# Optimization experiments

Hardware: AMD Instinct MI355X
Metric: run time of the kernel (lower is better)

The kernel has to match this reference:

```python
import jax, jax.numpy as jnp
import numpy as np

E = 2048      # enc_size
B = 64        # number of output buffer slices (leaves)
STEPS = 2 * B - 1  # 63 reduces then 64 shifts


def _res(x, W, b):
    # ResLayer: residual + ReLU MLP, x: (E,)
    return x + jax.nn.relu(x @ W + b)


def setup_inputs() -> dict:
    key = jax.random.key(0)
    ks = jax.random.split(key, 12)
    s = 1.0 / np.sqrt(E)
    inp = {
        "input_encoding": jax.random.normal(ks[0], (E,), dtype=jnp.float32),
        # 63 ones (reduce) followed by 64 zeros (shift): valid shift-reduce tree
        "fixed_actions": jnp.concatenate([jnp.ones((B - 1,), jnp.int64 if jax.config.jax_enable_x64 else jnp.int32),
                                          jnp.zeros((B,), jnp.int64 if jax.config.jax_enable_x64 else jnp.int32)]),
        # act_scorer: ResLayer + Linear(E, 2)
        "act_res_W": jax.random.normal(ks[1], (E, E), jnp.float32) * s,
        "act_res_b": jnp.zeros((E,), jnp.float32),
        "act_W": jax.random.normal(ks[2], (E, 2), jnp.float32) * s,
        "act_b": jnp.zeros((2,), jnp.float32),
        # unreduce_l: two ResLayers
        "ul1_W": jax.random.normal(ks[3], (E, E), jnp.float32) * s,
        "ul1_b": jnp.zeros((E,), jnp.float32),
        "ul2_W": jax.random.normal(ks[4], (E, E), jnp.float32) * s,
        "ul2_b": jnp.zeros((E,), jnp.float32),
        # unreduce_r: two ResLayers
        "ur1_W": jax.random.normal(ks[5], (E, E), jnp.float32) * s,
        "ur1_b": jnp.zeros((E,), jnp.float32),
        "ur2_W": jax.random.normal(ks[6], (E, E), jnp.float32) * s,
        "ur2_b": jnp.zeros((E,), jnp.float32),
    }
    return inp


def reference(input_encoding, act_res_W, act_res_b, act_W, act_b,
              ul1_W, ul1_b, ul2_W, ul2_b, ur1_W, ur1_b, ur2_W, ur2_b,
              fixed_actions):
    # fixed_actions is a constant action sequence -> Python-level unroll of the
    # data-dependent stack machine (faithful to the torch while-loop).
    acts = np.asarray(fixed_actions)
    stack = [input_encoding]
    buffer_slices = []
    logit_rec = []
    for step in range(acts.shape[0]):
        a = int(acts[step])
        top = stack[-1]
        logits = _res(top, act_res_W, act_res_b) @ act_W + act_b  # (2,)
        score = jax.nn.softmax(logits)[a]
        st = 1.0 + score - jax.lax.stop_gradient(score)  # straight-through scale (fwd == 1)
        logit_rec.append(logits)
        if a == 0:  # shift: pop to buffer
            x = stack.pop()
            buffer_slices.append(x * st)
            if len(stack) == 0:
                break
        else:  # reduce: pop, push unreduce_r then unreduce_l
            prev = stack.pop()
            l = _res(_res(prev, ul1_W, ul1_b), ul2_W, ul2_b)
            r = _res(_res(prev, ur1_W, ur1_b), ur2_W, ur2_b)
            stack.append(r * st)
            stack.append(l * st)
    return jnp.stack(buffer_slices, 0), jnp.stack(logit_rec, 0)
```

## Files before the change

kernel.cpp:

```cpp
#include <hip/hip_runtime.h>

#define EN 2048
#define NCH 256
#define CTH 1024
#define SENT 0xFFFFFFFFu

#define T_OFF    0
#define H_OFF    (64 * EN)
#define FLG_OFF  (128 * EN)
#define HT_OFF   (129 * EN)
#define P_OFF    (256 * EN)

#define AL64(p)   __hip_atomic_load((const unsigned long long*)(p), __ATOMIC_RELAXED, __HIP_MEMORY_SCOPE_AGENT)
#define AL32(p)   __hip_atomic_load((const unsigned*)(p), __ATOMIC_RELAXED, __HIP_MEMORY_SCOPE_AGENT)
#define AS32(p,v) __hip_atomic_store((unsigned*)(p), (v), __ATOMIC_RELAXED, __HIP_MEMORY_SCOPE_AGENT)
#define AS64(p,v) __hip_atomic_store((unsigned long long*)(p), (v), __ATOMIC_RELAXED, __HIP_MEMORY_SCOPE_AGENT)

__device__ __forceinline__ float af(unsigned u) { return __uint_as_float(u); }
__device__ __forceinline__ unsigned long long pk(float a, float b) {
    return ((unsigned long long)__float_as_uint(b) << 32) | __float_as_uint(a);
}

__device__ __forceinline__ void done_bar(unsigned* D, int b, int tid) {
    __syncthreads();
    if (tid < 64) {
        if (tid == 0) {
            asm volatile("s_waitcnt vmcnt(0)" ::: "memory");
            AS32(&D[b], 1u);
        }
        const unsigned long long* f = (const unsigned long long*)D;
        const unsigned long long GOOD = 0x0000000100000001ULL;
        for (long it = 0; it < 200000000L; ++it) {
            unsigned long long a = AL64(&f[tid * 2]);
            unsigned long long c = AL64(&f[tid * 2 + 1]);
            if (!__any((int)(a != GOOD || c != GOOD))) break;
        }
    }
    __syncthreads();
}

template<int NKT>
__device__ __forceinline__ void gemm_phase(
    const float* __restrict__ a_stage_row,
    const float* __restrict__ W, int kbase, int c0,
    float* __restrict__ Pslot, int tid, float* __restrict__ GB)
{
    const int kq  = tid >> 8;
    const int rem = tid & 255;
    const int ar  = rem >> 2;
    const int ak8 = (rem & 3) * 8;
    const int wk  = rem >> 3;
    const int wc  = (rem & 7) * 8;
    const int tr  = rem >> 4;
    const int tc  = rem & 15;
    float* As = GB + kq * (2 * 32 * 68);
    float* Wt = As + 32 * 68;

    float4 a0 = {0,0,0,0}, a1 = {0,0,0,0}, a2 = {0,0,0,0}, a3 = {0,0,0,0};

    unsigned long long ra0, ra1, ra2, ra3;
    float4 rw0, rw1;
    {
        ra0 = AL64(a_stage_row + kbase + ak8);
        ra1 = AL64(a_stage_row + kbase + ak8 + 2);
        ra2 = AL64(a_stage_row + kbase + ak8 + 4);
        ra3 = AL64(a_stage_row + kbase + ak8 + 6);
        const float* wp = W + (size_t)(kbase + wk) * EN + c0 + wc;
        rw0 = *(const float4*)wp; rw1 = *(const float4*)(wp + 4);
    }
    for (int kt = 0; kt < NKT; ++kt) {
        __syncthreads();
        As[(ak8+0)*68+ar] = af((unsigned)ra0); As[(ak8+1)*68+ar] = af((unsigned)(ra0>>32));
        As[(ak8+2)*68+ar] = af((unsigned)ra1); As[(ak8+3)*68+ar] = af((unsigned)(ra1>>32));
        As[(ak8+4)*68+ar] = af((unsigned)ra2); As[(ak8+5)*68+ar] = af((unsigned)(ra2>>32));
        As[(ak8+6)*68+ar] = af((unsigned)ra3); As[(ak8+7)*68+ar] = af((unsigned)(ra3>>32));
        *(float4*)&Wt[wk*68+wc]     = rw0;
        *(float4*)&Wt[wk*68+wc+4]  = rw1;
        __syncthreads();
        if (kt + 1 < NKT) {
            int kb = kbase + (kt + 1) * 32;
            ra0 = AL64(a_stage_row + kb + ak8);
            ra1 = AL64(a_stage_row + kb + ak8 + 2);
            ra2 = AL64(a_stage_row + kb + ak8 + 4);
            ra3 = AL64(a_stage_row + kb + ak8 + 6);
            const float* wp = W + (size_t)(kb + wk) * EN + c0 + wc;
            rw0 = *(const float4*)wp; rw1 = *(const float4*)(wp + 4);
        }
#pragma unroll
        for (int kk = 0; kk < 32; ++kk) {
            float4 av = *(const float4*)&As[kk*68 + tr*4];
            float4 wv = *(const float4*)&Wt[kk*68 + tc*4];
            a0.x += av.x*wv.x; a0.y += av.x*wv.y; a0.z += av.x*wv.z; a0.w += av.x*wv.w;
            a1.x += av.y*wv.x; a1.y += av.y*wv.y; a1.z += av.y*wv.z; a1.w += av.y*wv.w;
            a2.x += av.z*wv.x; a2.y += av.z*wv.y; a2.z += av.z*wv.z; a2.w += av.z*wv.w;
            a3.x += av.w*wv.x; a3.y += av.w*wv.y; a3.z += av.w*wv.z; a3.w += av.w*wv.w;
        }
    }
    __syncthreads();
    if (kq > 0) {
        float* d = GB + (kq - 1) * 4096 + rem;
        d[0*256]=a0.x; d[1*256]=a0.y; d[2*256]=a0.z;  d[3*256]=a0.w;
        d[4*256]=a1.x; d[5*256]=a1.y; d[6*256]=a1.z;  d[7*256]=a1.w;
        d[8*256]=a2.x; d[9*256]=a2.y; d[10*256]=a2.z; d[11*256]=a2.w;
        d[12*256]=a3.x; d[13*256]=a3.y; d[14*256]=a3.z; d[15*256]=a3.w;
    }
    __syncthreads();
    if (kq == 0) {
#pragma unroll
        for (int q = 0; q < 3; ++q) {
            const float* s = GB + q * 4096 + rem;
            a0.x+=s[0*256]; a0.y+=s[1*256]; a0.z+=s[2*256];  a0.w+=s[3*256];
            a1.x+=s[4*256]; a1.y+=s[5*256]; a1.z+=s[6*256];  a1.w+=s[7*256];
            a2.x+=s[8*256]; a2.y+=s[9*256]; a2.z+=s[10*256]; a2.w+=s[11*256];
            a3.x+=s[12*256]; a3.y+=s[13*256]; a3.z+=s[14*256]; a3.w+=s[15*256];
        }
        float* p0 = Pslot + (size_t)(tr*4    ) * EN + c0 + tc*4;
        float* p1 = Pslot + (size_t)(tr*4 + 1) * EN + c0 + tc*4;
        float* p2 = Pslot + (size_t)(tr*4 + 2) * EN + c0 + tc*4;
        float* p3 = Pslot + (size_t)(tr*4 + 3) * EN + c0 + tc*4;
        AS64(p0, pk(a0.x, a0.y)); AS64(p0 + 2, pk(a0.z, a0.w));
        AS64(p1, pk(a1.x, a1.y)); AS64(p1 + 2, pk(a1.z, a1.w));
        AS64(p2, pk(a2.x, a2.y)); AS64(p2 + 2, pk(a2.z, a2.w));
        AS64(p3, pk(a3.x, a3.y)); AS64(p3 + 2, pk(a3.z, a3.w));
    }
    __syncthreads();
}

__global__ __launch_bounds__(CTH, 1) void mega_kernel(
    const float* __restrict__ x0,
    const float* __restrict__ ul1W, const float* __restrict__ ul1b,
    const float* __restrict__ ul2W, const float* __restrict__ ul2b,
    const float* __restrict__ ur1W, const float* __restrict__ ur1b,
    const float* __restrict__ ur2W, const float* __restrict__ ur2b,
    const float* __restrict__ arW,  const float* __restrict__ arb,
    const float* __restrict__ aW,   const float* __restrict__ ab,
    float* __restrict__ T, float* __restrict__ Hb, float* __restrict__ RT1,
    float* __restrict__ HT, float* __restrict__ P, unsigned* __restrict__ FLG,
    float* __restrict__ out)
{
    __shared__ __align__(16) float xs[EN];
    __shared__ __align__(16) float red_t[16][20];
    __shared__ float bias_s[16];
    __shared__ __align__(16) float GB[4 * 2 * 32 * 68];
    __shared__ float lred[16][2];

    const int tid  = threadIdx.x;
    const int b    = blockIdx.x;
    const int lane = tid & 63;
    const int wv   = tid >> 6;

    {
        const int half  = b >> 7;
        const int idx   = b & 127;
        const int c0    = idx * 16;
        const int col   = tid & 15;
        const int chunk = tid >> 4;
        const float* Wg = half ? ul2W : ul1W;
        const float* bg = half ? ul2b : ul1b;

        float4 w[8];
#pragma unroll
        for (int j = 0; j < 8; ++j) {
            const float* wp = Wg + (size_t)(chunk * 32 + j * 4) * EN + c0 + col;
            w[j].x = wp[0]; w[j].y = wp[EN]; w[j].z = wp[2 * EN]; w[j].w = wp[3 * EN];
        }
        if (tid < 16) bias_s[tid] = bg[c0 + tid];

        for (int k = 1; k <= 63; ++k) {
            if (half == 0 && k == 1) {
                reinterpret_cast<float2*>(xs)[tid] = reinterpret_cast<const float2*>(x0)[tid];
            } else {
                const float* src = half ? (Hb + (size_t)k * EN) : (T + (size_t)(k - 1) * EN);
                const unsigned long long* s64 =
                    reinterpret_cast<const unsigned long long*>(src) + (size_t)wv * 64 + lane;
                unsigned long long v;
                for (;;) {
                    v = AL64(s64);
                    unsigned lo = (unsigned)v, hi = (unsigned)(v >> 32);
                    if (!__any((int)(lo == SENT || hi == SENT))) break;
                }
                float2 xv;
                xv.x = af((unsigned)v); xv.y = af((unsigned)(v >> 32));
                reinterpret_cast<float2*>(xs)[tid] = xv;
            }
            __syncthreads();

            float s = 0.f;
            const float4* xv4 = reinterpret_cast<const float4*>(xs) + chunk * 8;
#pragma unroll
            for (int j = 0; j < 8; ++j) {
                float4 x4 = xv4[j];
                s += x4.x * w[j].x + x4.y * w[j].y + x4.z * w[j].z + x4.w * w[j].w;
            }
            s += __shfl_xor(s, 16, 64);
            s += __shfl_xor(s, 32, 64);
            if (lane < 16) red_t[lane][wv] = s;
            __syncthreads();

            if (wv == 0 && lane < 16) {
                float4 r0 = *(const float4*)&red_t[lane][0];
                float4 r1 = *(const float4*)&red_t[lane][4];
                float4 r2 = *(const float4*)&red_t[lane][8];
                float4 r3 = *(const float4*)&red_t[lane][12];
                float tot = ((r0.x + r0.y) + (r0.z + r0.w)) + ((r1.x + r1.y) + (r1.z + r1.w))
                          + ((r2.x + r2.y) + (r2.z + r2.w)) + ((r3.x + r3.y) + (r3.z + r3.w))
                          + bias_s[lane];
                float o = xs[c0 + lane] + fmaxf(tot, 0.f);
                float* dst = half ? (T + (size_t)k * EN) : (Hb + (size_t)k * EN);
                AS32(&dst[c0 + lane], __float_as_uint(o));
                if (half && k == 63) out[c0 + lane] = o;
                if (!half && k == 1) AS32(&T[c0 + lane], __float_as_uint(xs[c0 + lane]));
            }
        }
    }

    unsigned* D0 = FLG;            unsigned* D1 = FLG + 256;
    unsigned* D2 = FLG + 512;      unsigned* D3 = FLG + 768;
    unsigned* D4 = FLG + 1024;     unsigned* D5 = FLG + 1280;

    {
        const int rem = tid & 255, kq = tid >> 8;
        int ar = rem >> 2; if (ar > 62) ar = 62;
        int cc = b & 31, ks = b >> 5;
        gemm_phase<2>(T + (size_t)ar * EN, ur1W, ks * 256 + kq * 64, cc * 64,
                      P + (size_t)ks * 64 * EN, tid, GB);
    }
    done_bar(D0, b, tid);

    if (tid < 504) {
        int m = tid >> 3, c = 8 * b + (tid & 7);
        float p = 0.f;
#pragma unroll
        for (int ks = 0; ks < 8; ++ks) p += af(AL32(P + ((size_t)ks * 64 + m) * EN + c));
        float tv = af(AL32(T + (size_t)m * EN + c));
        AS32(RT1 + (size_t)m * EN + c, __float_as_uint(tv + fmaxf(p + ur1b[c], 0.f)));
    }
    done_bar(D1, b, tid);

    {
        const int rem = tid & 255, kq = tid >> 8;
        int ar = rem >> 2; if (ar > 62) ar = 62;
        int cc = b & 31, ks = b >> 5;
        gemm_phase<2>(RT1 + (size_t)ar * EN, ur2W, ks * 256 + kq * 64, cc * 64,
                      P + (size_t)ks * 64 * EN, tid, GB);
    }
    done_bar(D2, b, tid);

    if (tid < 504) {
        int m = tid >> 3, c = 8 * b + (tid & 7);
        float p = 0.f;
#pragma unroll
        for (int ks = 0; ks < 8; ++ks) p += af(AL32(P + ((size_t)ks * 64 + m) * EN + c));
        float rv = af(AL32(RT1 + (size_t)m * EN + c));
        AS32(out + (size_t)(63 - m) * EN + c, __float_as_uint(rv + fmaxf(p + ur2b[c], 0.f)));
    }
    done_bar(D3, b, tid);

    {
        const int rem = tid & 255, kq = tid >> 8;
        int cc = b & 31, mh = (b >> 5) & 1, ks = b >> 6;
        int rp = mh * 64 + (rem >> 2); if (rp > 126) rp = 126;
        const float* arow = (rp <= 63) ? (T + (size_t)rp * EN) : (out + (size_t)(rp - 63) * EN);
        gemm_phase<4>(arow, arW, ks * 512 + kq * 128, cc * 64,
                      P + (size_t)(ks * 2 + mh) * 64 * EN, tid, GB);
    }
    done_bar(D4, b, tid);

    if (tid < 1016) {
        int m = tid >> 3, c = 8 * b + (tid & 7);
        int mh = m >> 6, mr = m & 63;
        float p = 0.f;
#pragma unroll
        for (int ks = 0; ks < 4; ++ks) p += af(AL32(P + ((size_t)(ks * 2 + mh) * 64 + mr) * EN + c));
        float tv = (m <= 63) ? af(AL32(T + (size_t)m * EN + c))
                             : af(AL32(out + (size_t)(m - 63) * EN + c));
        AS32(HT + (size_t)m * EN + c, __float_as_uint(tv + fmaxf(p + arb[c], 0.f)));
    }
    done_bar(D5, b, tid);

    if (b < 127) {
        const float* h = HT + (size_t)b * EN;
        unsigned long long hv = AL64(h + tid * 2);
        float h0 = af((unsigned)hv), h1 = af((unsigned)(hv >> 32));
        float4 w4 = *(const float4*)(aW + (size_t)tid * 4);
        float s0 = h0 * w4.x + h1 * w4.z;
        float s1 = h0 * w4.y + h1 * w4.w;
#pragma unroll
        for (int off = 32; off; off >>= 1) { s0 += __shfl_down(s0, off, 64); s1 += __shfl_down(s1, off, 64); }
        if (lane == 0) { lred[wv][0] = s0; lred[wv][1] = s1; }
        __syncthreads();
        if (tid == 0) {
            float t0 = ab[0], t1 = ab[1];
#pragma unroll
            for (int q = 0; q < 16; ++q) { t0 += lred[q][0]; t1 += lred[q][1]; }
            out[64 * EN + b * 2]     = t0;
            out[64 * EN + b * 2 + 1] = t1;
        }
    }
}

extern "C" void kernel_launch(void* const* d_in, const int* in_sizes, int n_in,
                              void* d_out, int out_size, void* d_ws, size_t ws_size,
                              hipStream_t stream)
{
    const float* x0   = (const float*)d_in[0];
    const float* arW  = (const float*)d_in[2];
    const float* arb  = (const float*)d_in[3];
    const float* aW   = (const float*)d_in[4];
    const float* ab   = (const float*)d_in[5];
    const float* ul1W = (const float*)d_in[6];
    const float* ul1b = (const float*)d_in[7];
    const float* ul2W = (const float*)d_in[8];
    const float* ul2b = (const float*)d_in[9];
    const float* ur1W = (const float*)d_in[10];
    const float* ur1b = (const float*)d_in[11];
    const float* ur2W = (const float*)d_in[12];
    const float* ur2b = (const float*)d_in[13];

    float* ws  = (float*)d_ws;
    float* out = (float*)d_out;
    float* T   = ws + T_OFF;
    float* Hb  = ws + H_OFF;
    float* RT1 = ws + H_OFF;
    float* HT  = ws + HT_OFF;
    float* P   = ws + P_OFF;
    unsigned* FLG = (unsigned*)(ws + FLG_OFF);

    hipMemsetAsync(ws, 0xFF, (size_t)(129 * EN) * sizeof(float), stream);

    void* args[] = { (void*)&x0, (void*)&ul1W, (void*)&ul1b, (void*)&ul2W, (void*)&ul2b,
                     (void*)&ur1W, (void*)&ur1b, (void*)&ur2W, (void*)&ur2b,
                     (void*)&arW, (void*)&arb, (void*)&aW, (void*)&ab,
                     (void*)&T, (void*)&Hb, (void*)&RT1, (void*)&HT, (void*)&P,
                     (void*)&FLG, (void*)&out };
    hipError_t err = hipLaunchCooperativeKernel(reinterpret_cast<void*>(mega_kernel),
                                                dim3(NCH), dim3(CTH), args, 0, stream);
    if (err != hipSuccess) {
        (void)hipGetLastError();
        mega_kernel<<<dim3(NCH), dim3(CTH), 0, stream>>>(
            x0, ul1W, ul1b, ul2W, ul2b, ur1W, ur1b, ur2W, ur2b,
            arW, arb, aW, ab, T, Hb, RT1, HT, P, FLG, out);
    }
}
```

Measured before the change: 359.0 us.

## Replace per-step syncthreads with LDS counter wait and vectorize cross-block loads

The serial unreduce_l chain now drops both per-step __syncthreads: waves bump a workgroup-scope LDS counter and only wave 0 spins on it before doing the final reduction, cutting barrier cost on the 63-step critical path. The split-K epilogue phases switch from scalar 32-bit atomic loads and stores to 16-byte loads and stores through inline asm with sc1, using fewer threads. The GEMM staging drops its register prefetch in favour of direct dwordx4 loads followed by a waitcnt. Risks include a race on xs reuse without a barrier, and the loss of load/compute overlap in the GEMM.

```diff
diff --git a/kernel.cpp b/kernel.cpp
--- a/kernel.cpp
+++ b/kernel.cpp
@@ -4,6 +4,9 @@
 #define NCH 256
 #define CTH 1024
 #define SENT 0xFFFFFFFFu
+
+typedef float f32x4 __attribute__((ext_vector_type(4)));
+typedef float f32x2 __attribute__((ext_vector_type(2)));
 
 #define T_OFF    0
 #define H_OFF    (64 * EN)
@@ -12,22 +15,18 @@
 #define P_OFF    (256 * EN)
 
 #define AL64(p)   __hip_atomic_load((const unsigned long long*)(p), __ATOMIC_RELAXED, __HIP_MEMORY_SCOPE_AGENT)
-#define AL32(p)   __hip_atomic_load((const unsigned*)(p), __ATOMIC_RELAXED, __HIP_MEMORY_SCOPE_AGENT)
 #define AS32(p,v) __hip_atomic_store((unsigned*)(p), (v), __ATOMIC_RELAXED, __HIP_MEMORY_SCOPE_AGENT)
-#define AS64(p,v) __hip_atomic_store((unsigned long long*)(p), (v), __ATOMIC_RELAXED, __HIP_MEMORY_SCOPE_AGENT)
+
+#define GL16(d, p) asm volatile("global_load_dwordx4 %0, %1, off sc1" : "=&v"(d) : "v"(p) : "memory")
+#define ST16(p, d) asm volatile("global_store_dwordx4 %0, %1, off sc1" :: "v"(p), "v"(d) : "memory")
 
 __device__ __forceinline__ float af(unsigned u) { return __uint_as_float(u); }
-__device__ __forceinline__ unsigned long long pk(float a, float b) {
-    return ((unsigned long long)__float_as_uint(b) << 32) | __float_as_uint(a);
-}
 
 __device__ __forceinline__ void done_bar(unsigned* D, int b, int tid) {
+    asm volatile("s_waitcnt vmcnt(0)" ::: "memory");
     __syncthreads();
     if (tid < 64) {
-        if (tid == 0) {
-            asm volatile("s_waitcnt vmcnt(0)" ::: "memory");
-            AS32(&D[b], 1u);
-        }
+        if (tid == 0) AS32(&D[b], 1u);
         const unsigned long long* f = (const unsigned long long*)D;
         const unsigned long long GOOD = 0x0000000100000001ULL;
         for (long it = 0; it < 200000000L; ++it) {
@@ -40,88 +39,70 @@
 }
 
 template<int NKT>
-__device__ __forceinline__ void gemm_phase(
-    const float* __restrict__ a_stage_row,
+__device__ __forceinline__ void gemm64(
+    const float* __restrict__ Arow,
     const float* __restrict__ W, int kbase, int c0,
     float* __restrict__ Pslot, int tid, float* __restrict__ GB)
 {
     const int kq  = tid >> 8;
     const int rem = tid & 255;
-    const int ar  = rem >> 2;
+    const int am  = rem >> 2;
     const int ak8 = (rem & 3) * 8;
     const int wk  = rem >> 3;
-    const int wc  = (rem & 7) * 8;
-    const int tr  = rem >> 4;
-    const int tc  = rem & 15;
-    float* As = GB + kq * (2 * 32 * 68);
-    float* Wt = As + 32 * 68;
-
-    float4 a0 = {0,0,0,0}, a1 = {0,0,0,0}, a2 = {0,0,0,0}, a3 = {0,0,0,0};
-
-    unsigned long long ra0, ra1, ra2, ra3;
-    float4 rw0, rw1;
-    {
-        ra0 = AL64(a_stage_row + kbase + ak8);
-        ra1 = AL64(a_stage_row + kbase + ak8 + 2);
-        ra2 = AL64(a_stage_row + kbase + ak8 + 4);
-        ra3 = AL64(a_stage_row + kbase + ak8 + 6);
-        const float* wp = W + (size_t)(kbase + wk) * EN + c0 + wc;
-        rw0 = *(const float4*)wp; rw1 = *(const float4*)(wp + 4);
-    }
+    const int wq  = rem & 7;
+    const int tr  = rem >> 4, tc = rem & 15;
+    float* As = GB + kq * 4352;
+    float* Wt = As + 2176;
+
+    f32x4 acc0 = (f32x4)(0.f), acc1 = (f32x4)(0.f), acc2 = (f32x4)(0.f), acc3 = (f32x4)(0.f);
+
     for (int kt = 0; kt < NKT; ++kt) {
+        int kb = kbase + kt * 32;
+        f32x4 ra0, ra1;
+        GL16(ra0, Arow + kb + ak8);
+        GL16(ra1, Arow + kb + ak8 + 4);
+        const float* wp = W + (size_t)(kb + wk) * EN + c0 + wq * 8;
+        f32x4 rw0 = *(const f32x4*)wp;
+        f32x4 rw1 = *(const f32x4*)(wp + 4);
+        asm volatile("s_waitcnt vmcnt(0)" : "+v"(ra0), "+v"(ra1) :: "memory");
         __syncthreads();
-        As[(ak8+0)*68+ar] = af((unsigned)ra0); As[(ak8+1)*68+ar] = af((unsigned)(ra0>>32));
-        As[(ak8+2)*68+ar] = af((unsigned)ra1); As[(ak8+3)*68+ar] = af((unsigned)(ra1>>32));
-        As[(ak8+4)*68+ar] = af((unsigned)ra2); As[(ak8+5)*68+ar] = af((unsigned)(ra2>>32));
-        As[(ak8+6)*68+ar] = af((unsigned)ra3); As[(ak8+7)*68+ar] = af((unsigned)(ra3>>32));
-        *(float4*)&Wt[wk*68+wc]     = rw0;
-        *(float4*)&Wt[wk*68+wc+4]  = rw1;
+        As[(ak8 + 0) * 68 + am] = ra0.x; As[(ak8 + 1) * 68 + am] = ra0.y;
+        As[(ak8 + 2) * 68 + am] = ra0.z; As[(ak8 + 3) * 68 + am] = ra0.w;
+        As[(ak8 + 4) * 68 + am] = ra1.x; As[(ak8 + 5) * 68 + am] = ra1.y;
+        As[(ak8 + 6) * 68 + am] = ra1.z; As[(ak8 + 7) * 68 + am] = ra1.w;
+        *(f32x4*)&Wt[wk * 68 + wq * 8]     = rw0;
+        *(f32x4*)&Wt[wk * 68 + wq * 8 + 4] = rw1;
         __syncthreads();
-        if (kt + 1 < NKT) {
-            int kb = kbase + (kt + 1) * 32;
-            ra0 = AL64(a_stage_row + kb + ak8);
-            ra1 = AL64(a_stage_row + kb + ak8 + 2);
-            ra2 = AL64(a_stage_row + kb + ak8 + 4);
-            ra3 = AL64(a_stage_row + kb + ak8 + 6);
-            const float* wp = W + (size_t)(kb + wk) * EN + c0 + wc;
-            rw0 = *(const float4*)wp; rw1 = *(const float4*)(wp + 4);
-        }
 #pragma unroll
         for (int kk = 0; kk < 32; ++kk) {
-            float4 av = *(const float4*)&As[kk*68 + tr*4];
-            float4 wv = *(const float4*)&Wt[kk*68 + tc*4];
-            a0.x += av.x*wv.x; a0.y += av.x*wv.y; a0.z += av.x*wv.z; a0.w += av.x*wv.w;
-            a1.x += av.y*wv.x; a1.y += av.y*wv.y; a1.z += av.y*wv.z; a1.w += av.y*wv.w;
-            a2.x += av.z*wv.x; a2.y += av.z*wv.y; a2.z += av.z*wv.z; a2.w += av.z*wv.w;
-            a3.x += av.w*wv.x; a3.y += av.w*wv.y; a3.z += av.w*wv.z; a3.w += av.w*wv.w;
-        }
-    }
-    __syncthreads();
-    if (kq > 0) {
-        float* d = GB + (kq - 1) * 4096 + rem;
-        d[0*256]=a0.x; d[1*256]=a0.y; d[2*256]=a0.z;  d[3*256]=a0.w;
-        d[4*256]=a1.x; d[5*256]=a1.y; d[6*256]=a1.z;  d[7*256]=a1.w;
-        d[8*256]=a2.x; d[9*256]=a2.y; d[10*256]=a2.z; d[11*256]=a2.w;
-        d[12*256]=a3.x; d[13*256]=a3.y; d[14*256]=a3.z; d[15*256]=a3.w;
+            f32x4 av  = *(const f32x4*)&As[kk * 68 + tr * 4];
+            f32x4 wv4 = *(const f32x4*)&Wt[kk * 68 + tc * 4];
+            acc0 += av.x * wv4; acc1 += av.y * wv4;
+            acc2 += av.z * wv4; acc3 += av.w * wv4;
+        }
+    }
+    __syncthreads();
+    if (kq) {
+        float* d = GB + (kq - 1) * 4352 + rem;
+        d[0*256]=acc0.x;  d[1*256]=acc0.y;  d[2*256]=acc0.z;  d[3*256]=acc0.w;
+        d[4*256]=acc1.x;  d[5*256]=acc1.y;  d[6*256]=acc1.z;  d[7*256]=acc1.w;
+        d[8*256]=acc2.x;  d[9*256]=acc2.y;  d[10*256]=acc2.z; d[11*256]=acc2.w;
+        d[12*256]=acc3.x; d[13*256]=acc3.y; d[14*256]=acc3.z; d[15*256]=acc3.w;
     }
     __syncthreads();
     if (kq == 0) {
 #pragma unroll
         for (int q = 0; q < 3; ++q) {
-            const float* s = GB + q * 4096 + rem;
-            a0.x+=s[0*256]; a0.y+=s[1*256]; a0.z+=s[2*256];  a0.w+=s[3*256];
-            a1.x+=s[4*256]; a1.y+=s[5*256]; a1.z+=s[6*256];  a1.w+=s[7*256];
-            a2.x+=s[8*256]; a2.y+=s[9*256]; a2.z+=s[10*256]; a2.w+=s[11*256];
-            a3.x+=s[12*256]; a3.y+=s[13*256]; a3.z+=s[14*256]; a3.w+=s[15*256];
-        }
-        float* p0 = Pslot + (size_t)(tr*4    ) * EN + c0 + tc*4;
-        float* p1 = Pslot + (size_t)(tr*4 + 1) * EN + c0 + tc*4;
-        float* p2 = Pslot + (size_t)(tr*4 + 2) * EN + c0 + tc*4;
-        float* p3 = Pslot + (size_t)(tr*4 + 3) * EN + c0 + tc*4;
-        AS64(p0, pk(a0.x, a0.y)); AS64(p0 + 2, pk(a0.z, a0.w));
-        AS64(p1, pk(a1.x, a1.y)); AS64(p1 + 2, pk(a1.z, a1.w));
-        AS64(p2, pk(a2.x, a2.y)); AS64(p2 + 2, pk(a2.z, a2.w));
-        AS64(p3, pk(a3.x, a3.y)); AS64(p3 + 2, pk(a3.z, a3.w));
+            const float* s = GB + q * 4352 + rem;
+            acc0.x+=s[0*256];  acc0.y+=s[1*256];  acc0.z+=s[2*256];  acc0.w+=s[3*256];
+            acc1.x+=s[4*256];  acc1.y+=s[5*256];  acc1.z+=s[6*256];  acc1.w+=s[7*256];
+            acc2.x+=s[8*256];  acc2.y+=s[9*256];  acc2.z+=s[10*256]; acc2.w+=s[11*256];
+            acc3.x+=s[12*256]; acc3.y+=s[13*256]; acc3.z+=s[14*256]; acc3.w+=s[15*256];
+        }
+        ST16(Pslot + (size_t)(tr * 4 + 0) * EN + c0 + tc * 4, acc0);
+        ST16(Pslot + (size_t)(tr * 4 + 1) * EN + c0 + tc * 4, acc1);
+        ST16(Pslot + (size_t)(tr * 4 + 2) * EN + c0 + tc * 4, acc2);
+        ST16(Pslot + (size_t)(tr * 4 + 3) * EN + c0 + tc * 4, acc3);
     }
     __syncthreads();
 }
@@ -141,8 +122,9 @@
     __shared__ __align__(16) float xs[EN];
     __shared__ __align__(16) float red_t[16][20];
     __shared__ float bias_s[16];
-    __shared__ __align__(16) float GB[4 * 2 * 32 * 68];
+    __shared__ __align__(16) float GB[4 * 4352];
     __shared__ float lred[16][2];
+    __shared__ unsigned cnt;
 
     const int tid  = threadIdx.x;
     const int b    = blockIdx.x;
@@ -158,17 +140,19 @@
         const float* Wg = half ? ul2W : ul1W;
         const float* bg = half ? ul2b : ul1b;
 
-        float4 w[8];
+        f32x4 w[8];
 #pragma unroll
         for (int j = 0; j < 8; ++j) {
             const float* wp = Wg + (size_t)(chunk * 32 + j * 4) * EN + c0 + col;
             w[j].x = wp[0]; w[j].y = wp[EN]; w[j].z = wp[2 * EN]; w[j].w = wp[3 * EN];
         }
         if (tid < 16) bias_s[tid] = bg[c0 + tid];
+        if (tid == 0) cnt = 0;
+        __syncthreads();
 
         for (int k = 1; k <= 63; ++k) {
             if (half == 0 && k == 1) {
-                reinterpret_cast<float2*>(xs)[tid] = reinterpret_cast<const float2*>(x0)[tid];
+                reinterpret_cast<f32x2*>(xs)[tid] = reinterpret_cast<const f32x2*>(x0)[tid];
             } else {
                 const float* src = half ? (Hb + (size_t)k * EN) : (T + (size_t)(k - 1) * EN);
                 const unsigned long long* s64 =
@@ -179,102 +163,137 @@
                     unsigned lo = (unsigned)v, hi = (unsigned)(v >> 32);
                     if (!__any((int)(lo == SENT || hi == SENT))) break;
                 }
-                float2 xv;
-                xv.x = af((unsigned)v); xv.y = af((unsigned)(v >> 32));
-                reinterpret_cast<float2*>(xs)[tid] = xv;
+                f32x2 xv; xv.x = af((unsigned)v); xv.y = af((unsigned)(v >> 32));
+                reinterpret_cast<f32x2*>(xs)[tid] = xv;
             }
-            __syncthreads();
 
             float s = 0.f;
-            const float4* xv4 = reinterpret_cast<const float4*>(xs) + chunk * 8;
+            const f32x4* xv4 = reinterpret_cast<const f32x4*>(xs) + chunk * 8;
 #pragma unroll
             for (int j = 0; j < 8; ++j) {
-                float4 x4 = xv4[j];
+                f32x4 x4 = xv4[j];
                 s += x4.x * w[j].x + x4.y * w[j].y + x4.z * w[j].z + x4.w * w[j].w;
             }
             s += __shfl_xor(s, 16, 64);
             s += __shfl_xor(s, 32, 64);
             if (lane < 16) red_t[lane][wv] = s;
-            __syncthreads();
-
-            if (wv == 0 && lane < 16) {
-                float4 r0 = *(const float4*)&red_t[lane][0];
-                float4 r1 = *(const float4*)&red_t[lane][4];
-                float4 r2 = *(const float4*)&red_t[lane][8];
-                float4 r3 = *(const float4*)&red_t[lane][12];
-                float tot = ((r0.x + r0.y) + (r0.z + r0.w)) + ((r1.x + r1.y) + (r1.z + r1.w))
-                          + ((r2.x + r2.y) + (r2.z + r2.w)) + ((r3.x + r3.y) + (r3.z + r3.w))
-                          + bias_s[lane];
-                float o = xs[c0 + lane] + fmaxf(tot, 0.f);
-                float* dst = half ? (T + (size_t)k * EN) : (Hb + (size_t)k * EN);
-                AS32(&dst[c0 + lane], __float_as_uint(o));
-                if (half && k == 63) out[c0 + lane] = o;
-                if (!half && k == 1) AS32(&T[c0 + lane], __float_as_uint(xs[c0 + lane]));
+            if (lane == 0)
+                __hip_atomic_fetch_add(&cnt, 1u, __ATOMIC_RELEASE, __HIP_MEMORY_SCOPE_WORKGROUP);
+
+            if (wv == 0) {
+                unsigned tgt = 16u * (unsigned)k;
+                while (__hip_atomic_load(&cnt, __ATOMIC_ACQUIRE, __HIP_MEMORY_SCOPE_WORKGROUP) < tgt) {}
+                if (lane < 16) {
+                    f32x4 r0 = *(const f32x4*)&red_t[lane][0];
+                    f32x4 r1 = *(const f32x4*)&red_t[lane][4];
+                    f32x4 r2 = *(const f32x4*)&red_t[lane][8];
+                    f32x4 r3 = *(const f32x4*)&red_t[lane][12];
+                    float tot = ((r0.x + r0.y) + (r0.z + r0.w)) + ((r1.x + r1.y) + (r1.z + r1.w))
+                              + ((r2.x + r2.y) + (r2.z + r2.w)) + ((r3.x + r3.y) + (r3.z + r3.w))
+                              + bias_s[lane];
+                    float o = xs[c0 + lane] + fmaxf(tot, 0.f);
+                    float* dst = half ? (T + (size_t)k * EN) : (Hb + (size_t)k * EN);
+                    AS32(&dst[c0 + lane], __float_as_uint(o));
+                    if (half && k == 63) out[c0 + lane] = o;
+                    if (!half && k == 1) AS32(&T[c0 + lane], __float_as_uint(xs[c0 + lane]));
+                }
             }
         }
     }
 
-    unsigned* D0 = FLG;            unsigned* D1 = FLG + 256;
-    unsigned* D2 = FLG + 512;      unsigned* D3 = FLG + 768;
-    unsigned* D4 = FLG + 1024;     unsigned* D5 = FLG + 1280;
+    unsigned* D0 = FLG;        unsigned* D1 = FLG + 256;  unsigned* D2 = FLG + 512;
+    unsigned* D3 = FLG + 768;  unsigned* D4 = FLG + 1024; unsigned* D5 = FLG + 1280;
+    const int rem = tid & 255;
+    const int sar = rem >> 2;
 
     {
-        const int rem = tid & 255, kq = tid >> 8;
-        int ar = rem >> 2; if (ar > 62) ar = 62;
-        int cc = b & 31, ks = b >> 5;
-        gemm_phase<2>(T + (size_t)ar * EN, ur1W, ks * 256 + kq * 64, cc * 64,
-                      P + (size_t)ks * 64 * EN, tid, GB);
+        int cc = b & 31, ks = b >> 5, kq = tid >> 8;
+        int ar = sar > 62 ? 62 : sar;
+        gemm64<2>(T + (size_t)ar * EN, ur1W, ks * 256 + kq * 64, cc * 64,
+                  P + (size_t)ks * 64 * EN, tid, GB);
     }
     done_bar(D0, b, tid);
 
-    if (tid < 504) {
-        int m = tid >> 3, c = 8 * b + (tid & 7);
-        float p = 0.f;
-#pragma unroll
-        for (int ks = 0; ks < 8; ++ks) p += af(AL32(P + ((size_t)ks * 64 + m) * EN + c));
-        float tv = af(AL32(T + (size_t)m * EN + c));
-        AS32(RT1 + (size_t)m * EN + c, __float_as_uint(tv + fmaxf(p + ur1b[c], 0.f)));
+    if (tid < 126) {
+        int m = tid >> 1, qd = tid & 1;
+        int c = 8 * b + qd * 4;
+        const float* pc = P + (size_t)m * EN + c;
+        f32x4 v0, v1, v2, v3, v4, v5, v6, v7, tv;
+        GL16(v0, pc + (size_t)0 * 64 * EN); GL16(v1, pc + (size_t)1 * 64 * EN);
+        GL16(v2, pc + (size_t)2 * 64 * EN); GL16(v3, pc + (size_t)3 * 64 * EN);
+        GL16(v4, pc + (size_t)4 * 64 * EN); GL16(v5, pc + (size_t)5 * 64 * EN);
+        GL16(v6, pc + (size_t)6 * 64 * EN); GL16(v7, pc + (size_t)7 * 64 * EN);
+        GL16(tv, T + (size_t)m * EN + c);
+        asm volatile("s_waitcnt vmcnt(0)"
+            : "+v"(v0),"+v"(v1),"+v"(v2),"+v"(v3),"+v"(v4),"+v"(v5),"+v"(v6),"+v"(v7),"+v"(tv)
+            :: "memory");
+        f32x4 sum = ((v0 + v1) + (v2 + v3)) + ((v4 + v5) + (v6 + v7));
+        f32x4 bb = *(const f32x4*)(ur1b + c);
+        f32x4 r;
+        r.x = tv.x + fmaxf(sum.x + bb.x, 0.f); r.y = tv.y + fmaxf(sum.y + bb.y, 0.f);
+        r.z = tv.z + fmaxf(sum.z + bb.z, 0.f); r.w = tv.w + fmaxf(sum.w + bb.w, 0.f);
+        ST16(RT1 + (size_t)m * EN + c, r);
     }
     done_bar(D1, b, tid);
 
     {
-        const int rem = tid & 255, kq = tid >> 8;
-        int ar = rem >> 2; if (ar > 62) ar = 62;
-        int cc = b & 31, ks = b >> 5;
-        gemm_phase<2>(RT1 + (size_t)ar * EN, ur2W, ks * 256 + kq * 64, cc * 64,
-                      P + (size_t)ks * 64 * EN, tid, GB);
+        int cc = b & 31, ks = b >> 5, kq = tid >> 8;
+        int ar = sar > 62 ? 62 : sar;
+        gemm64<2>(RT1 + (size_t)ar * EN, ur2W, ks * 256 + kq * 64, cc * 64,
+                  P + (size_t)ks * 64 * EN, tid, GB);
     }
     done_bar(D2, b, tid);
 
-    if (tid < 504) {
-        int m = tid >> 3, c = 8 * b + (tid & 7);
-        float p = 0.f;
-#pragma unroll
-        for (int ks = 0; ks < 8; ++ks) p += af(AL32(P + ((size_t)ks * 64 + m) * EN + c));
-        float rv = af(AL32(RT1 + (size_t)m * EN + c));
-        AS32(out + (size_t)(63 - m) * EN + c, __float_as_uint(rv + fmaxf(p + ur2b[c], 0.f)));
+    if (tid < 126) {
+        int m = tid >> 1, qd = tid & 1;
+        int c = 8 * b + qd * 4;
+        const float* pc = P + (size_t)m * EN + c;
+        f32x4 v0, v1, v2, v3, v4, v5, v6, v7, tv;
+        GL16(v0, pc + (size_t)0 * 64 * EN); GL16(v1, pc + (size_t)1 * 64 * EN);
+        GL16(v2, pc + (size_t)2 * 64 * EN); GL16(v3, pc + (size_t)3 * 64 * EN);
+        GL16(v4, pc + (size_t)4 * 64 * EN); GL16(v5, pc + (size_t)5 * 64 * EN);
+        GL16(v6, pc + (size_t)6 * 64 * EN); GL16(v7, pc + (size_t)7 * 64 * EN);
+        GL16(tv, RT1 + (size_t)m * EN + c);
+        asm volatile("s_waitcnt vmcnt(0)"
+            : "+v"(v0),"+v"(v1),"+v"(v2),"+v"(v3),"+v"(v4),"+v"(v5),"+v"(v6),"+v"(v7),"+v"(tv)
+            :: "memory");
+        f32x4 sum = ((v0 + v1) + (v2 + v3)) + ((v4 + v5) + (v6 + v7));
+        f32x4 bb = *(const f32x4*)(ur2b + c);
+        f32x4 r;
+        r.x = tv.x + fmaxf(sum.x + bb.x, 0.f); r.y = tv.y + fmaxf(sum.y + bb.y, 0.f);
+        r.z = tv.z + fmaxf(sum.z + bb.z, 0.f); r.w = tv.w + fmaxf(sum.w + bb.w, 0.f);
+        ST16(out + (size_t)(63 - m) * EN + c, r);
     }
     done_bar(D3, b, tid);
 
     {
-        const int rem = tid & 255, kq = tid >> 8;
-        int cc = b & 31, mh = (b >> 5) & 1, ks = b >> 6;
-        int rp = mh * 64 + (rem >> 2); if (rp > 126) rp = 126;
+        int cc = b & 31, mh = (b >> 5) & 1, ks = b >> 6, kq = tid >> 8;
+        int rp = mh * 64 + sar; if (rp > 126) rp = 126;
         const float* arow = (rp <= 63) ? (T + (size_t)rp * EN) : (out + (size_t)(rp - 63) * EN);
-        gemm_phase<4>(arow, arW, ks * 512 + kq * 128, cc * 64,
-                      P + (size_t)(ks * 2 + mh) * 64 * EN, tid, GB);
+        gemm64<4>(arow, arW, ks * 512 + kq * 128, cc * 64,
+                  P + (size_t)(ks * 2 + mh) * 64 * EN, tid, GB);
     }
     done_bar(D4, b, tid);
 
-    if (tid < 1016) {
-        int m = tid >> 3, c = 8 * b + (tid & 7);
+    if (tid < 254) {
+        int m = tid >> 1, qd = tid & 1;
+        int c = 8 * b + qd * 4;
         int mh = m >> 6, mr = m & 63;
-        float p = 0.f;
-#pragma unroll
-        for (int ks = 0; ks < 4; ++ks) p += af(AL32(P + ((size_t)(ks * 2 + mh) * 64 + mr) * EN + c));
-        float tv = (m <= 63) ? af(AL32(T + (size_t)m * EN + c))
-                             : af(AL32(out + (size_t)(m - 63) * EN + c));
-        AS32(HT + (size_t)m * EN + c, __float_as_uint(tv + fmaxf(p + arb[c], 0.f)));
+        f32x4 v0, v1, v2, v3, tv;
+        GL16(v0, P + ((size_t)(0 * 2 + mh) * 64 + mr) * EN + c);
+        GL16(v1, P + ((size_t)(1 * 2 + mh) * 64 + mr) * EN + c);
+        GL16(v2, P + ((size_t)(2 * 2 + mh) * 64 + mr) * EN + c);
+        GL16(v3, P + ((size_t)(3 * 2 + mh) * 64 + mr) * EN + c);
+        const float* trow = (m <= 63) ? (T + (size_t)m * EN) : (out + (size_t)(m - 63) * EN);
+        GL16(tv, trow + c);
+        asm volatile("s_waitcnt vmcnt(0)"
+            : "+v"(v0),"+v"(v1),"+v"(v2),"+v"(v3),"+v"(tv) :: "memory");
+        f32x4 sum = (v0 + v1) + (v2 + v3);
+        f32x4 bb = *(const f32x4*)(arb + c);
+        f32x4 r;
+        r.x = tv.x + fmaxf(sum.x + bb.x, 0.f); r.y = tv.y + fmaxf(sum.y + bb.y, 0.f);
+        r.z = tv.z + fmaxf(sum.z + bb.z, 0.f); r.w = tv.w + fmaxf(sum.w + bb.w, 0.f);
+        ST16(HT + (size_t)m * EN + c, r);
     }
     done_bar(D5, b, tid);
 
@@ -282,7 +301,7 @@
         const float* h = HT + (size_t)b * EN;
         unsigned long long hv = AL64(h + tid * 2);
         float h0 = af((unsigned)hv), h1 = af((unsigned)(hv >> 32));
-        float4 w4 = *(const float4*)(aW + (size_t)tid * 4);
+        f32x4 w4 = *(const f32x4*)(aW + (size_t)tid * 4);
         float s0 = h0 * w4.x + h1 * w4.z;
         float s1 = h0 * w4.y + h1 * w4.w;
 #pragma unroll
```

Measured after the change: 332.2 us. 1.08x faster.
